# Performance work log

Hardware: AMD Instinct MI355X
Metric: run time of the kernel (lower is better)

Reference implementation:

```python
import jax, jax.numpy as jnp
import numpy as np

B, CIN, COUT, N, K = 4, 64, 64, 16384, 8


def setup_inputs() -> dict:
    key = jax.random.key(0)
    k1, k2, k3, k4, k5 = jax.random.split(key, 5)
    features = jax.random.normal(k1, (B, CIN, N), dtype=jnp.float32)
    neighborhood = jax.random.randint(k2, (B, K, N), 0, N, dtype=jnp.int32)
    positions = jax.random.uniform(k3, (B, 3, N), dtype=jnp.float32)
    # learned parameters (kaiming-uniform-ish init)
    lim_t = np.sqrt(6.0 / CIN)
    weight_theta = jax.random.uniform(k4, (3, CIN, COUT), dtype=jnp.float32,
                                      minval=-lim_t, maxval=lim_t)
    weight_bias = jax.random.uniform(k5, (CIN, COUT), dtype=jnp.float32,
                                     minval=-lim_t, maxval=lim_t)
    bias = jnp.zeros((COUT,), dtype=jnp.float32)
    return {"features": features, "weight_theta": weight_theta,
            "weight_bias": weight_bias, "neighborhood": neighborhood,
            "positions": positions, "bias": bias}


def reference(features, weight_theta, weight_bias, neighborhood, positions, bias):
    # features: [B, Cin, N]; positions: [B, 3, N]; neighborhood: [B, K, N]
    Bv, Cin, Nv = features.shape
    Kv = neighborhood.shape[1]
    # gather neighbor positions: pos_j[b,d,k,n] = positions[b,d, nbh[b,k,n]]
    pos_j = jnp.take_along_axis(positions[:, :, None, :],
                                neighborhood[:, None, :, :].astype(jnp.int32),
                                axis=3)                        # [B,3,K,N]
    delta = pos_j - positions[:, :, None, :]                   # [B,3,K,N]
    # position-dependent linear weight applied to center features:
    # contrib[b,k,o,n] = sum_d delta[b,d,k,n] * (theta.f)[b,d,o,n] + (wb.f)[b,o,n]
    ft = jnp.einsum('dio,bin->bdon', weight_theta, features)   # [B,3,Cout,N]
    fb = jnp.einsum('io,bin->bon', weight_bias, features)      # [B,Cout,N]
    contrib = jnp.einsum('bdkn,bdon->bkon', delta, ft) + fb[:, None]  # [B,K,Cout,N]

    def scatter_b(contrib_b, idx_b):
        # contrib_b: [K,Cout,N], idx_b: [K,N]
        data = contrib_b.transpose(0, 2, 1).reshape(-1, contrib_b.shape[1])  # [K*N, Cout]
        ids = idx_b.reshape(-1)
        return jax.ops.segment_sum(data, ids, num_segments=Nv).T  # [Cout, N]

    out = jax.vmap(scatter_b)(contrib, neighborhood)           # [B,Cout,N]
    return out + bias[None, :, None]
```

## Files before the change

### kernel.cpp

```cpp
#include <hip/hip_runtime.h>
#include <hip/hip_fp16.h>

#define B_    4
#define CIN_  64
#define COUT_ 64
#define N_    16384
#define K_    8

#define EDGES_PER_B (K_ * N_)
#define TOT_EDGES   (B_ * EDGES_PER_B)


__global__ __launch_bounds__(256) void fc_hist(
    const int* __restrict__ nbh,
    int*       __restrict__ counts)
{
    const int gid = blockIdx.x * 256 + threadIdx.x;
    const int b   = gid / EDGES_PER_B;
    const int j   = nbh[gid];
    atomicAdd(&counts[b * N_ + j], 1);
}

__global__ __launch_bounds__(256) void fc_scan(
    const int* __restrict__ counts,
    int*       __restrict__ offsets,
    int*       __restrict__ cursor)
{
    __shared__ int s[256];
    const int b = blockIdx.x;
    const int t = threadIdx.x;
    const int base = b * N_ + t * 64;

    int sum = 0;
    #pragma unroll
    for (int e = 0; e < 64; ++e) sum += counts[base + e];
    s[t] = sum;
    __syncthreads();

    for (int d = 1; d < 256; d <<= 1) {
        const int v = (t >= d) ? s[t - d] : 0;
        __syncthreads();
        s[t] += v;
        __syncthreads();
    }

    int off = s[t] - sum;
    #pragma unroll
    for (int e = 0; e < 64; ++e) {
        const int c = counts[base + e];
        offsets[base + e] = off;
        cursor[base + e]  = off;
        off += c;
    }
}

__global__ __launch_bounds__(256) void fc_rec(
    const int*   __restrict__ nbh,
    const float* __restrict__ pos,
    int*         __restrict__ cursor,
    float4*      __restrict__ rec)
{
    const int gid = blockIdx.x * 256 + threadIdx.x;
    const int b   = gid >> 14;
    const int n   = gid & (N_ - 1);

    const int*   nbhb = nbh + (size_t)b * K_ * N_;
    const float* posb = pos + (size_t)b * 3 * N_;
    float4*      recb = rec + ((size_t)b * N_ + n) * K_;

    #pragma unroll
    for (int k = 0; k < K_; ++k) {
        const int j    = nbhb[k * N_ + n];
        const int slot = atomicAdd(&cursor[b * N_ + j], 1);
        const float qx = posb[j];
        const float qy = posb[N_ + j];
        const float qz = posb[2 * N_ + j];
        recb[k] = make_float4(qx, qy, qz, __int_as_float(slot));
    }
}


__global__ __launch_bounds__(512, 4) void fc_contribA(
    const float*  __restrict__ feat,
    const float*  __restrict__ theta,
    const float*  __restrict__ wbias,
    const float4* __restrict__ rec,
    const float*  __restrict__ pos,
    __half*       __restrict__ contrib)
{
    __shared__ float4 Wl[CIN_ * COUT_];
    __shared__ float  Fl[CIN_ * 64];

    const int tid  = threadIdx.x;
    const int lane = tid & 63;
    const int w    = tid >> 6;

    const int blocks_per_b = N_ / 128;
    const int b     = blockIdx.x / blocks_per_b;
    const int nbase = (blockIdx.x % blocks_per_b) * 128;

    for (int e = tid; e < CIN_ * COUT_; e += 512) {
        const int i = e >> 6, o = e & 63;
        float4 wv;
        wv.x = theta[0 * CIN_ * COUT_ + i * COUT_ + o];
        wv.y = theta[1 * CIN_ * COUT_ + i * COUT_ + o];
        wv.z = theta[2 * CIN_ * COUT_ + i * COUT_ + o];
        wv.w = wbias[i * COUT_ + o];
        Wl[e] = wv;
    }

    const float*  featb = feat + (size_t)b * CIN_ * N_;
    const float*  posb  = pos  + (size_t)b * 3 * N_;
    const float4* recb  = rec  + (size_t)b * N_ * K_;
    __half*       cb    = contrib + ((size_t)b * EDGES_PER_B << 6);

    for (int t = 0; t < 2; ++t) {
        const int n0 = nbase + t * 64;

        __syncthreads();
        for (int r = 0; r < 8; ++r) {
            const int i = r * 8 + w;
            Fl[i * 64 + lane] = featb[(size_t)i * N_ + n0 + lane];
        }
        __syncthreads();

        const int nn = w * 8;
        float4 acc[8];
        #pragma unroll
        for (int j = 0; j < 8; ++j) acc[j] = make_float4(0.f, 0.f, 0.f, 0.f);

        #pragma unroll 2
        for (int i = 0; i < CIN_; ++i) {
            const float4 wv = Wl[i * 64 + lane];
            const float4 fA = *(const float4*)&Fl[i * 64 + nn];
            const float4 fB = *(const float4*)&Fl[i * 64 + nn + 4];
            const float fs[8] = {fA.x, fA.y, fA.z, fA.w, fB.x, fB.y, fB.z, fB.w};
            #pragma unroll
            for (int j = 0; j < 8; ++j) {
                acc[j].x = fmaf(wv.x, fs[j], acc[j].x);
                acc[j].y = fmaf(wv.y, fs[j], acc[j].y);
                acc[j].z = fmaf(wv.z, fs[j], acc[j].z);
                acc[j].w = fmaf(wv.w, fs[j], acc[j].w);
            }
        }

        #pragma unroll
        for (int j = 0; j < 8; ++j) {
            const int n = n0 + nn + j;
            const float px = posb[0 * N_ + n];
            const float py = posb[1 * N_ + n];
            const float pz = posb[2 * N_ + n];
            float4 a = acc[j];
            a.w = fmaf(-px, a.x, fmaf(-py, a.y, fmaf(-pz, a.z, a.w)));
            #pragma unroll
            for (int k = 0; k < K_; ++k) {
                const float4 r = recb[(size_t)n * K_ + k];
                const int slot = __float_as_int(r.w);
                const float c  = fmaf(r.x, a.x, fmaf(r.y, a.y, fmaf(r.z, a.z, a.w)));
                cb[((size_t)slot << 6) + lane] = __float2half(c);
            }
        }
    }
}

struct h4 { __half2 lo, hi; };

__global__ __launch_bounds__(512) void fc_gatherA(
    const __half* __restrict__ contrib,
    const int*    __restrict__ offsets,
    const int*    __restrict__ counts,
    const float*  __restrict__ bias,
    float*        __restrict__ out)
{
    __shared__ float T[64][65];
    __shared__ float V[64][65];
    const int tid  = threadIdx.x;
    const int lane = tid & 63;
    const int w    = tid >> 6;

    const int tiles_per_b = N_ / 64;
    const int b  = blockIdx.x / tiles_per_b;
    const int n0 = (blockIdx.x % tiles_per_b) * 64;

    const __half* cb  = contrib + ((size_t)b * EDGES_PER_B << 6);
    const h4*     cb4 = (const h4*)cb;

    for (int g = 0; g < 8; ++g) {
        const int jj = w * 8 + g;
        const int j  = n0 + jj;
        const int base = offsets[b * N_ + j];
        const int cnt  = counts[b * N_ + j];

        const h4* p4 = cb4 + ((size_t)base << 4) + (lane >> 4) * 16 + (lane & 15);
        float2 sl = make_float2(0.f, 0.f);
        float2 sh = make_float2(0.f, 0.f);
        const int full = cnt >> 2;
        int it = 0;
        for (; it + 2 <= full; it += 2) {
            const h4 a0 = p4[0];
            const h4 a1 = p4[64];
            float2 t0 = __half22float2(a0.lo), t1 = __half22float2(a1.lo);
            sl.x += t0.x + t1.x; sl.y += t0.y + t1.y;
            t0 = __half22float2(a0.hi); t1 = __half22float2(a1.hi);
            sh.x += t0.x + t1.x; sh.y += t0.y + t1.y;
            p4 += 128;
        }
        if (it < full) {
            const h4 a0 = p4[0];
            float2 t0 = __half22float2(a0.lo);
            sl.x += t0.x; sl.y += t0.y;
            t0 = __half22float2(a0.hi);
            sh.x += t0.x; sh.y += t0.y;
        }
        sl.x += __shfl_xor(sl.x, 16); sl.y += __shfl_xor(sl.y, 16);
        sh.x += __shfl_xor(sh.x, 16); sh.y += __shfl_xor(sh.y, 16);
        sl.x += __shfl_xor(sl.x, 32); sl.y += __shfl_xor(sl.y, 32);
        sh.x += __shfl_xor(sh.x, 32); sh.y += __shfl_xor(sh.y, 32);

        float tail = 0.f;
        const __half* pt = cb + (((size_t)(base + (full << 2))) << 6) + lane;
        for (int e = full << 2; e < cnt; ++e) { tail += __half2float(*pt); pt += 64; }

        T[jj][lane] = tail;
        if (lane < 16) {
            V[jj][4 * lane + 0] = sl.x;
            V[jj][4 * lane + 1] = sl.y;
            V[jj][4 * lane + 2] = sh.x;
            V[jj][4 * lane + 3] = sh.y;
        }
    }
    __syncthreads();

    float* outb = out + (size_t)b * COUT_ * N_;
    for (int r = 0; r < 8; ++r) {
        const int o = r * 8 + w;
        outb[(size_t)o * N_ + n0 + lane] = T[lane][o] + V[lane][o] + bias[o];
    }
}


__global__ __launch_bounds__(256) void fc_fill_slot(
    const int* __restrict__ nbh,
    int*       __restrict__ cursor,
    int*       __restrict__ slotmap)
{
    const int gid = blockIdx.x * 256 + threadIdx.x;
    const int b   = gid / EDGES_PER_B;
    const int j   = nbh[gid];
    slotmap[gid] = atomicAdd(&cursor[b * N_ + j], 1);
}

__global__ __launch_bounds__(256) void fc_contrib(
    const float* __restrict__ feat,
    const float* __restrict__ theta,
    const float* __restrict__ wbias,
    const int*   __restrict__ nbh,
    const int*   __restrict__ slotmap,
    const float* __restrict__ pos,
    float*       __restrict__ contrib)
{
    __shared__ float4 Wl[CIN_ * COUT_];
    __shared__ float  Fl[CIN_ * 64];

    const int tid  = threadIdx.x;
    const int lane = tid & 63;
    const int w    = tid >> 6;

    const int blocks_per_b = N_ / 128;
    const int b     = blockIdx.x / blocks_per_b;
    const int nbase = (blockIdx.x % blocks_per_b) * 128;

    for (int e = tid; e < CIN_ * COUT_; e += 256) {
        const int i = e >> 6, o = e & 63;
        float4 wv;
        wv.x = theta[0 * CIN_ * COUT_ + i * COUT_ + o];
        wv.y = theta[1 * CIN_ * COUT_ + i * COUT_ + o];
        wv.z = theta[2 * CIN_ * COUT_ + i * COUT_ + o];
        wv.w = wbias[i * COUT_ + o];
        Wl[e] = wv;
    }

    const float* featb = feat + (size_t)b * CIN_ * N_;
    const float* posb  = pos  + (size_t)b * 3 * N_;
    const int*   nbhb  = nbh  + (size_t)b * K_ * N_;
    const int*   smb   = slotmap + (size_t)b * EDGES_PER_B;
    float*       cb    = contrib + ((size_t)b * EDGES_PER_B << 6);

    for (int t = 0; t < 2; ++t) {
        const int n0 = nbase + t * 64;

        __syncthreads();
        for (int r = 0; r < 16; ++r) {
            const int i = r * 4 + w;
            Fl[i * 64 + lane] = featb[(size_t)i * N_ + n0 + lane];
        }
        __syncthreads();

        for (int g = 0; g < 4; ++g) {
            const int nn = w * 16 + g * 4;
            float4 acc[4];
            #pragma unroll
            for (int j = 0; j < 4; ++j) acc[j] = make_float4(0.f, 0.f, 0.f, 0.f);

            #pragma unroll 8
            for (int i = 0; i < CIN_; ++i) {
                const float4 wv = Wl[i * 64 + lane];
                const float f0 = Fl[i * 64 + nn + 0];
                const float f1 = Fl[i * 64 + nn + 1];
                const float f2 = Fl[i * 64 + nn + 2];
                const float f3 = Fl[i * 64 + nn + 3];
                acc[0].x = fmaf(wv.x, f0, acc[0].x);
                acc[0].y = fmaf(wv.y, f0, acc[0].y);
                acc[0].z = fmaf(wv.z, f0, acc[0].z);
                acc[0].w = fmaf(wv.w, f0, acc[0].w);
                acc[1].x = fmaf(wv.x, f1, acc[1].x);
                acc[1].y = fmaf(wv.y, f1, acc[1].y);
                acc[1].z = fmaf(wv.z, f1, acc[1].z);
                acc[1].w = fmaf(wv.w, f1, acc[1].w);
                acc[2].x = fmaf(wv.x, f2, acc[2].x);
                acc[2].y = fmaf(wv.y, f2, acc[2].y);
                acc[2].z = fmaf(wv.z, f2, acc[2].z);
                acc[2].w = fmaf(wv.w, f2, acc[2].w);
                acc[3].x = fmaf(wv.x, f3, acc[3].x);
                acc[3].y = fmaf(wv.y, f3, acc[3].y);
                acc[3].z = fmaf(wv.z, f3, acc[3].z);
                acc[3].w = fmaf(wv.w, f3, acc[3].w);
            }

            #pragma unroll
            for (int j = 0; j < 4; ++j) {
                const int n = n0 + nn + j;
                const float px = posb[0 * N_ + n];
                const float py = posb[1 * N_ + n];
                const float pz = posb[2 * N_ + n];
                float4 a = acc[j];
                a.w = fmaf(-px, a.x, fmaf(-py, a.y, fmaf(-pz, a.z, a.w)));
                #pragma unroll
                for (int k = 0; k < K_; ++k) {
                    const int jt   = nbhb[k * N_ + n];
                    const int slot = smb[k * N_ + n];
                    const float qx = posb[0 * N_ + jt];
                    const float qy = posb[1 * N_ + jt];
                    const float qz = posb[2 * N_ + jt];
                    const float c  = fmaf(qx, a.x, fmaf(qy, a.y, fmaf(qz, a.z, a.w)));
                    cb[((size_t)slot << 6) + lane] = c;
                }
            }
        }
    }
}

__global__ __launch_bounds__(512) void fc_gather3(
    const float* __restrict__ contrib,
    const int*   __restrict__ offsets,
    const int*   __restrict__ counts,
    const float* __restrict__ bias,
    float*       __restrict__ out)
{
    __shared__ float T[64][65];
    const int tid  = threadIdx.x;
    const int lane = tid & 63;
    const int w    = tid >> 6;

    const int tiles_per_b = N_ / 64;
    const int b  = blockIdx.x / tiles_per_b;
    const int n0 = (blockIdx.x % tiles_per_b) * 64;

    const float* cb = contrib + ((size_t)b * EDGES_PER_B << 6);

    for (int g = 0; g < 8; ++g) {
        const int jj = w * 8 + g;
        const int j  = n0 + jj;
        const int base = offsets[b * N_ + j];
        const int cnt  = counts[b * N_ + j];

        const float* p = cb + ((size_t)base << 6) + lane;
        float acc = 0.f;
        int e = 0;
        for (; e + 4 <= cnt; e += 4) {
            const float v0 = p[0];
            const float v1 = p[64];
            const float v2 = p[128];
            const float v3 = p[192];
            acc += (v0 + v1) + (v2 + v3);
            p += 256;
        }
        for (; e < cnt; ++e) { acc += *p; p += 64; }
        T[jj][lane] = acc;
    }
    __syncthreads();

    float* outb = out + (size_t)b * COUT_ * N_;
    for (int r = 0; r < 8; ++r) {
        const int o = r * 8 + w;
        outb[(size_t)o * N_ + n0 + lane] = T[lane][o] + bias[o];
    }
}

__global__ __launch_bounds__(256) void flexconv_main(
    const float* __restrict__ feat,
    const float* __restrict__ theta,
    const float* __restrict__ wbias,
    const int*   __restrict__ nbh,
    const float* __restrict__ pos,
    float*       __restrict__ ws)
{
    __shared__ float4 Wl[CIN_ * COUT_];
    __shared__ float  Fl[CIN_ * 64];

    const int tid  = threadIdx.x;
    const int lane = tid & 63;
    const int w    = tid >> 6;

    const int blocks_per_b = N_ / 128;
    const int b     = blockIdx.x / blocks_per_b;
    const int nbase = (blockIdx.x % blocks_per_b) * 128;

    for (int e = tid; e < CIN_ * COUT_; e += 256) {
        const int i = e >> 6, o = e & 63;
        float4 wv;
        wv.x = theta[0 * CIN_ * COUT_ + i * COUT_ + o];
        wv.y = theta[1 * CIN_ * COUT_ + i * COUT_ + o];
        wv.z = theta[2 * CIN_ * COUT_ + i * COUT_ + o];
        wv.w = wbias[i * COUT_ + o];
        Wl[e] = wv;
    }

    const float* featb = feat + (size_t)b * CIN_ * N_;
    const float* posb  = pos  + (size_t)b * 3 * N_;
    const int*   nbhb  = nbh  + (size_t)b * K_ * N_;
    float*       wsb   = ws   + (size_t)b * N_ * COUT_;

    for (int t = 0; t < 2; ++t) {
        const int n0 = nbase + t * 64;

        __syncthreads();
        for (int r = 0; r < 16; ++r) {
            const int i = r * 4 + w;
            Fl[i * 64 + lane] = featb[(size_t)i * N_ + n0 + lane];
        }
        __syncthreads();

        for (int g = 0; g < 4; ++g) {
            const int nn = w * 16 + g * 4;
            float4 acc[4];
            #pragma unroll
            for (int j = 0; j < 4; ++j) acc[j] = make_float4(0.f, 0.f, 0.f, 0.f);

            #pragma unroll 8
            for (int i = 0; i < CIN_; ++i) {
                const float4 wv = Wl[i * 64 + lane];
                const float f0 = Fl[i * 64 + nn + 0];
                const float f1 = Fl[i * 64 + nn + 1];
                const float f2 = Fl[i * 64 + nn + 2];
                const float f3 = Fl[i * 64 + nn + 3];
                acc[0].x = fmaf(wv.x, f0, acc[0].x);
                acc[0].y = fmaf(wv.y, f0, acc[0].y);
                acc[0].z = fmaf(wv.z, f0, acc[0].z);
                acc[0].w = fmaf(wv.w, f0, acc[0].w);
                acc[1].x = fmaf(wv.x, f1, acc[1].x);
                acc[1].y = fmaf(wv.y, f1, acc[1].y);
                acc[1].z = fmaf(wv.z, f1, acc[1].z);
                acc[1].w = fmaf(wv.w, f1, acc[1].w);
                acc[2].x = fmaf(wv.x, f2, acc[2].x);
                acc[2].y = fmaf(wv.y, f2, acc[2].y);
                acc[2].z = fmaf(wv.z, f2, acc[2].z);
                acc[2].w = fmaf(wv.w, f2, acc[2].w);
                acc[3].x = fmaf(wv.x, f3, acc[3].x);
                acc[3].y = fmaf(wv.y, f3, acc[3].y);
                acc[3].z = fmaf(wv.z, f3, acc[3].z);
                acc[3].w = fmaf(wv.w, f3, acc[3].w);
            }

            #pragma unroll
            for (int j = 0; j < 4; ++j) {
                const int n = n0 + nn + j;
                const float px = posb[0 * N_ + n];
                const float py = posb[1 * N_ + n];
                const float pz = posb[2 * N_ + n];
                const float4 a = acc[j];
                #pragma unroll
                for (int k = 0; k < K_; ++k) {
                    const int idx = nbhb[k * N_ + n];
                    const float dx = posb[0 * N_ + idx] - px;
                    const float dy = posb[1 * N_ + idx] - py;
                    const float dz = posb[2 * N_ + idx] - pz;
                    const float c  = fmaf(dx, a.x, fmaf(dy, a.y, fmaf(dz, a.z, a.w)));
                    atomicAdd(&wsb[(size_t)idx * COUT_ + lane], c);
                }
            }
        }
    }
}

__global__ __launch_bounds__(256) void flexconv_finish(
    const float* __restrict__ ws,
    const float* __restrict__ bias,
    float*       __restrict__ out)
{
    __shared__ float T[64][65];
    const int tid  = threadIdx.x;
    const int lane = tid & 63;
    const int w    = tid >> 6;

    const int tiles_per_b = N_ / 64;
    const int b  = blockIdx.x / tiles_per_b;
    const int n0 = (blockIdx.x % tiles_per_b) * 64;

    const float* wsb = ws + (size_t)b * N_ * COUT_;
    for (int r = 0; r < 16; ++r) {
        const int nn = r * 4 + w;
        T[nn][lane] = wsb[(size_t)(n0 + nn) * COUT_ + lane];
    }
    __syncthreads();

    float* outb = out + (size_t)b * COUT_ * N_;
    for (int r = 0; r < 16; ++r) {
        const int o = r * 4 + w;
        outb[(size_t)o * N_ + n0 + lane] = T[lane][o] + bias[o];
    }
}

extern "C" void kernel_launch(void* const* d_in, const int* in_sizes, int n_in,
                              void* d_out, int out_size, void* d_ws, size_t ws_size,
                              hipStream_t stream) {
    const float* features = (const float*)d_in[0];
    const float* theta    = (const float*)d_in[1];
    const float* wbias    = (const float*)d_in[2];
    const int*   nbh      = (const int*)  d_in[3];
    const float* pos      = (const float*)d_in[4];
    const float* bias     = (const float*)d_in[5];
    float* out = (float*)d_out;

    const size_t counts_bytes    = (size_t)B_ * N_ * sizeof(int);
    const size_t map_bytes       = (size_t)TOT_EDGES * sizeof(int);
    const size_t rec_bytes       = (size_t)TOT_EDGES * sizeof(float4);
    const size_t contribh_bytes  = (size_t)TOT_EDGES * COUT_ * sizeof(__half);
    const size_t contribf_bytes  = (size_t)TOT_EDGES * COUT_ * sizeof(float);

    {
        size_t off = 0;
        __half* contrib = (__half*)((char*)d_ws + off); off += contribh_bytes;
        int*    offsets = (int*)   ((char*)d_ws + off); off += counts_bytes;
        int*    counts  = (int*)   ((char*)d_ws + off); off += counts_bytes;
        int*    cursor  = (int*)   ((char*)d_ws + off); off += counts_bytes;
        float4* rec     = (float4*)((char*)d_ws + off); off += rec_bytes;

        if (ws_size >= off) {
            hipMemsetAsync(counts, 0, counts_bytes, stream);
            fc_hist<<<TOT_EDGES / 256, 256, 0, stream>>>(nbh, counts);
            fc_scan<<<B_, 256, 0, stream>>>(counts, offsets, cursor);
            fc_rec<<<(B_ * N_) / 256, 256, 0, stream>>>(nbh, pos, cursor, rec);
            fc_contribA<<<B_ * (N_ / 128), 512, 0, stream>>>(features, theta, wbias,
                                                             rec, pos, contrib);
            fc_gatherA<<<B_ * (N_ / 64), 512, 0, stream>>>(contrib, offsets, counts,
                                                           bias, out);
            return;
        }
    }

    {
        size_t off = 0;
        float* contrib = (float*)((char*)d_ws + off); off += contribf_bytes;
        int* counts  = (int*)((char*)d_ws + off); off += counts_bytes;
        int* offsets = (int*)((char*)d_ws + off); off += counts_bytes;
        int* cursor  = (int*)((char*)d_ws + off); off += counts_bytes;
        int* slotmap = (int*)((char*)d_ws + off); off += map_bytes;

        if (ws_size >= off) {
            hipMemsetAsync(counts, 0, counts_bytes, stream);
            fc_hist<<<TOT_EDGES / 256, 256, 0, stream>>>(nbh, counts);
            fc_scan<<<B_, 256, 0, stream>>>(counts, offsets, cursor);
            fc_fill_slot<<<TOT_EDGES / 256, 256, 0, stream>>>(nbh, cursor, slotmap);
            fc_contrib<<<B_ * (N_ / 128), 256, 0, stream>>>(features, theta, wbias,
                                                            nbh, slotmap, pos, contrib);
            fc_gather3<<<B_ * (N_ / 64), 512, 0, stream>>>(contrib, offsets, counts,
                                                           bias, out);
            return;
        }
    }

    {
        float* ws = (float*)d_ws;
        const size_t ws_bytes = (size_t)B_ * N_ * COUT_ * sizeof(float);
        hipMemsetAsync(ws, 0, ws_bytes, stream);
        flexconv_main<<<B_ * (N_ / 128), 256, 0, stream>>>(features, theta, wbias,
                                                           nbh, pos, ws);
        flexconv_finish<<<B_ * (N_ / 64), 256, 0, stream>>>(ws, bias, out);
    }
}
```

Baseline: 190.1 us.

## Fuse all stages into one cooperative persistent kernel with grid syncs

Replaces the memset plus five-kernel pipeline (histogram, scan, record build, contribution, gather) with a single cooperative kernel of 512 blocks. Stages are separated by grid.sync, so per-launch overhead and inter-kernel gaps go away. The gather stage reuses the weight tile's shared memory and handles two tiles per block. Drawbacks are a serial 4-block scan phase while the rest of the grid waits, plus the cost of each grid barrier. If the cooperative launch fails (for example, too many blocks to be co-resident), the code falls back to the old path. The unused fp32 slotmap path is also removed.

Result: slower. 467.3 us (+145.9%).

```diff
diff --git a/kernel.cpp b/kernel.cpp
--- a/kernel.cpp
+++ b/kernel.cpp
@@ -1,5 +1,8 @@
 #include <hip/hip_runtime.h>
 #include <hip/hip_fp16.h>
+#include <hip/hip_cooperative_groups.h>
+
+namespace cg = cooperative_groups;
 
 #define B_    4
 #define CIN_  64
@@ -9,6 +12,228 @@
 
 #define EDGES_PER_B (K_ * N_)
 #define TOT_EDGES   (B_ * EDGES_PER_B)
+
+#define FB 512
+#define FT 512
+
+struct h4 { __half2 lo, hi; };
+
+__global__ __launch_bounds__(512, 4) void fc_fused(
+    const float*  __restrict__ feat,
+    const float*  __restrict__ theta,
+    const float*  __restrict__ wbias,
+    const int*    __restrict__ nbh,
+    const float*  __restrict__ pos,
+    const float*  __restrict__ bias,
+    float*        __restrict__ out,
+    __half*       __restrict__ contrib,
+    int*          __restrict__ offsets,
+    int*          __restrict__ counts,
+    int*          __restrict__ cursor,
+    float4*       __restrict__ rec)
+{
+    __shared__ float4 Wl[CIN_ * COUT_];
+    __shared__ float  Fl[CIN_ * 64];
+
+    cg::grid_group grid = cg::this_grid();
+
+    const int tid = threadIdx.x;
+    const int blk = blockIdx.x;
+    const int gid = blk * FT + tid;
+
+    if (gid < B_ * N_) counts[gid] = 0;
+    grid.sync();
+
+    #pragma unroll
+    for (int r = 0; r < 2; ++r) {
+        const int e = gid + r * (FB * FT);
+        const int b = e / EDGES_PER_B;
+        atomicAdd(&counts[b * N_ + nbh[e]], 1);
+    }
+    grid.sync();
+
+    if (blk < B_) {
+        int* s = (int*)Fl;
+        const int base = blk * N_ + tid * 32;
+        int sum = 0;
+        #pragma unroll
+        for (int q = 0; q < 32; ++q) sum += counts[base + q];
+        s[tid] = sum;
+        __syncthreads();
+        for (int d = 1; d < 512; d <<= 1) {
+            const int v = (tid >= d) ? s[tid - d] : 0;
+            __syncthreads();
+            s[tid] += v;
+            __syncthreads();
+        }
+        int off = s[tid] - sum;
+        #pragma unroll
+        for (int q = 0; q < 32; ++q) {
+            const int c = counts[base + q];
+            offsets[base + q] = off;
+            cursor [base + q] = off;
+            off += c;
+        }
+    }
+    grid.sync();
+
+    if (gid < B_ * N_) {
+        const int b = gid >> 14;
+        const int n = gid & (N_ - 1);
+        const int*   nbhb = nbh + (size_t)b * K_ * N_;
+        const float* posb = pos + (size_t)b * 3 * N_;
+        float4*      recb = rec + ((size_t)b * N_ + n) * K_;
+        #pragma unroll
+        for (int k = 0; k < K_; ++k) {
+            const int j    = nbhb[k * N_ + n];
+            const int slot = atomicAdd(&cursor[b * N_ + j], 1);
+            recb[k] = make_float4(posb[j], posb[N_ + j], posb[2 * N_ + j],
+                                  __int_as_float(slot));
+        }
+    }
+    grid.sync();
+
+    {
+        const int lane = tid & 63;
+        const int w    = tid >> 6;
+        const int b     = blk >> 7;
+        const int nbase = (blk & 127) * 128;
+
+        for (int e = tid; e < CIN_ * COUT_; e += FT) {
+            const int i = e >> 6, o = e & 63;
+            float4 wv;
+            wv.x = theta[0 * CIN_ * COUT_ + i * COUT_ + o];
+            wv.y = theta[1 * CIN_ * COUT_ + i * COUT_ + o];
+            wv.z = theta[2 * CIN_ * COUT_ + i * COUT_ + o];
+            wv.w = wbias[i * COUT_ + o];
+            Wl[e] = wv;
+        }
+
+        const float*  featb = feat + (size_t)b * CIN_ * N_;
+        const float*  posb  = pos  + (size_t)b * 3 * N_;
+        const float4* recb  = rec  + (size_t)b * N_ * K_;
+        __half*       cb    = contrib + ((size_t)b * EDGES_PER_B << 6);
+
+        for (int t = 0; t < 2; ++t) {
+            const int n0 = nbase + t * 64;
+
+            __syncthreads();
+            for (int r = 0; r < 8; ++r) {
+                const int i = r * 8 + w;
+                Fl[i * 64 + lane] = featb[(size_t)i * N_ + n0 + lane];
+            }
+            __syncthreads();
+
+            const int nn = w * 8;
+            float4 acc[8];
+            #pragma unroll
+            for (int j = 0; j < 8; ++j) acc[j] = make_float4(0.f, 0.f, 0.f, 0.f);
+
+            #pragma unroll 2
+            for (int i = 0; i < CIN_; ++i) {
+                const float4 wv = Wl[i * 64 + lane];
+                const float4 fA = *(const float4*)&Fl[i * 64 + nn];
+                const float4 fB = *(const float4*)&Fl[i * 64 + nn + 4];
+                const float fs[8] = {fA.x, fA.y, fA.z, fA.w, fB.x, fB.y, fB.z, fB.w};
+                #pragma unroll
+                for (int j = 0; j < 8; ++j) {
+                    acc[j].x = fmaf(wv.x, fs[j], acc[j].x);
+                    acc[j].y = fmaf(wv.y, fs[j], acc[j].y);
+                    acc[j].z = fmaf(wv.z, fs[j], acc[j].z);
+                    acc[j].w = fmaf(wv.w, fs[j], acc[j].w);
+                }
+            }
+
+            #pragma unroll
+            for (int j = 0; j < 8; ++j) {
+                const int n = n0 + nn + j;
+                const float px = posb[0 * N_ + n];
+                const float py = posb[1 * N_ + n];
+                const float pz = posb[2 * N_ + n];
+                float4 a = acc[j];
+                a.w = fmaf(-px, a.x, fmaf(-py, a.y, fmaf(-pz, a.z, a.w)));
+                #pragma unroll
+                for (int k = 0; k < K_; ++k) {
+                    const float4 r = recb[(size_t)n * K_ + k];
+                    const int slot = __float_as_int(r.w);
+                    const float c  = fmaf(r.x, a.x, fmaf(r.y, a.y, fmaf(r.z, a.z, a.w)));
+                    cb[((size_t)slot << 6) + lane] = __float2half(c);
+                }
+            }
+        }
+    }
+    grid.sync();
+
+    {
+        float (*T)[65] = (float (*)[65])((char*)Wl);
+        float (*V)[65] = (float (*)[65])((char*)Wl + 64 * 65 * sizeof(float));
+        const int lane = tid & 63;
+        const int w    = tid >> 6;
+
+        for (int rep = 0; rep < 2; ++rep) {
+            const int vb = blk + rep * FB;
+            const int b  = vb >> 8;
+            const int n0 = (vb & 255) * 64;
+
+            const __half* cb  = contrib + ((size_t)b * EDGES_PER_B << 6);
+            const h4*     cb4 = (const h4*)cb;
+
+            __syncthreads();
+
+            for (int g = 0; g < 8; ++g) {
+                const int jj = w * 8 + g;
+                const int j  = n0 + jj;
+                const int base = offsets[b * N_ + j];
+                const int cnt  = counts[b * N_ + j];
+
+                const h4* p4 = cb4 + ((size_t)base << 4) + (lane >> 4) * 16 + (lane & 15);
+                float2 sl = make_float2(0.f, 0.f);
+                float2 sh = make_float2(0.f, 0.f);
+                const int full = cnt >> 2;
+                int it = 0;
+                for (; it + 2 <= full; it += 2) {
+                    const h4 a0 = p4[0];
+                    const h4 a1 = p4[64];
+                    float2 t0 = __half22float2(a0.lo), t1 = __half22float2(a1.lo);
+                    sl.x += t0.x + t1.x; sl.y += t0.y + t1.y;
+                    t0 = __half22float2(a0.hi); t1 = __half22float2(a1.hi);
+                    sh.x += t0.x + t1.x; sh.y += t0.y + t1.y;
+                    p4 += 128;
+                }
+                if (it < full) {
+                    const h4 a0 = p4[0];
+                    float2 t0 = __half22float2(a0.lo);
+                    sl.x += t0.x; sl.y += t0.y;
+                    t0 = __half22float2(a0.hi);
+                    sh.x += t0.x; sh.y += t0.y;
+                }
+                sl.x += __shfl_xor(sl.x, 16); sl.y += __shfl_xor(sl.y, 16);
+                sh.x += __shfl_xor(sh.x, 16); sh.y += __shfl_xor(sh.y, 16);
+                sl.x += __shfl_xor(sl.x, 32); sl.y += __shfl_xor(sl.y, 32);
+                sh.x += __shfl_xor(sh.x, 32); sh.y += __shfl_xor(sh.y, 32);
+
+                float tail = 0.f;
+                const __half* pt = cb + (((size_t)(base + (full << 2))) << 6) + lane;
+                for (int e = full << 2; e < cnt; ++e) { tail += __half2float(*pt); pt += 64; }
+
+                T[jj][lane] = tail;
+                if (lane < 16) {
+                    V[jj][4 * lane + 0] = sl.x;
+                    V[jj][4 * lane + 1] = sl.y;
+                    V[jj][4 * lane + 2] = sh.x;
+                    V[jj][4 * lane + 3] = sh.y;
+                }
+            }
+            __syncthreads();
+
+            float* outb = out + (size_t)b * COUT_ * N_;
+            for (int r = 0; r < 8; ++r) {
+                const int o = r * 8 + w;
+                outb[(size_t)o * N_ + n0 + lane] = T[lane][o] + V[lane][o] + bias[o];
+            }
+        }
+    }
+}
 
 
 __global__ __launch_bounds__(256) void fc_hist(
@@ -72,13 +297,10 @@
     for (int k = 0; k < K_; ++k) {
         const int j    = nbhb[k * N_ + n];
         const int slot = atomicAdd(&cursor[b * N_ + j], 1);
-        const float qx = posb[j];
-        const float qy = posb[N_ + j];
-        const float qz = posb[2 * N_ + j];
-        recb[k] = make_float4(qx, qy, qz, __int_as_float(slot));
-    }
-}
-
+        recb[k] = make_float4(posb[j], posb[N_ + j], posb[2 * N_ + j],
+                              __int_as_float(slot));
+    }
+}
 
 __global__ __launch_bounds__(512, 4) void fc_contribA(
     const float*  __restrict__ feat,
@@ -163,8 +385,6 @@
     }
 }
 
-struct h4 { __half2 lo, hi; };
-
 __global__ __launch_bounds__(512) void fc_gatherA(
     const __half* __restrict__ contrib,
     const int*    __restrict__ offsets,
@@ -238,26 +458,13 @@
     }
 }
 
-
-__global__ __launch_bounds__(256) void fc_fill_slot(
-    const int* __restrict__ nbh,
-    int*       __restrict__ cursor,
-    int*       __restrict__ slotmap)
-{
-    const int gid = blockIdx.x * 256 + threadIdx.x;
-    const int b   = gid / EDGES_PER_B;
-    const int j   = nbh[gid];
-    slotmap[gid] = atomicAdd(&cursor[b * N_ + j], 1);
-}
-
-__global__ __launch_bounds__(256) void fc_contrib(
+__global__ __launch_bounds__(256) void flexconv_main(
     const float* __restrict__ feat,
     const float* __restrict__ theta,
     const float* __restrict__ wbias,
     const int*   __restrict__ nbh,
-    const int*   __restrict__ slotmap,
     const float* __restrict__ pos,
-    float*       __restrict__ contrib)
+    float*       __restrict__ ws)
 {
     __shared__ float4 Wl[CIN_ * COUT_];
     __shared__ float  Fl[CIN_ * 64];
@@ -283,8 +490,7 @@
     const float* featb = feat + (size_t)b * CIN_ * N_;
     const float* posb  = pos  + (size_t)b * 3 * N_;
     const int*   nbhb  = nbh  + (size_t)b * K_ * N_;
-    const int*   smb   = slotmap + (size_t)b * EDGES_PER_B;
-    float*       cb    = contrib + ((size_t)b * EDGES_PER_B << 6);
+    float*       wsb   = ws   + (size_t)b * N_ * COUT_;
 
     for (int t = 0; t < 2; ++t) {
         const int n0 = nbase + t * 64;
@@ -333,151 +539,6 @@
                 const float px = posb[0 * N_ + n];
                 const float py = posb[1 * N_ + n];
                 const float pz = posb[2 * N_ + n];
-                float4 a = acc[j];
-                a.w = fmaf(-px, a.x, fmaf(-py, a.y, fmaf(-pz, a.z, a.w)));
-                #pragma unroll
-                for (int k = 0; k < K_; ++k) {
-                    const int jt   = nbhb[k * N_ + n];
-                    const int slot = smb[k * N_ + n];
-                    const float qx = posb[0 * N_ + jt];
-                    const float qy = posb[1 * N_ + jt];
-                    const float qz = posb[2 * N_ + jt];
-                    const float c  = fmaf(qx, a.x, fmaf(qy, a.y, fmaf(qz, a.z, a.w)));
-                    cb[((size_t)slot << 6) + lane] = c;
-                }
-            }
-        }
-    }
-}
-
-__global__ __launch_bounds__(512) void fc_gather3(
-    const float* __restrict__ contrib,
-    const int*   __restrict__ offsets,
-    const int*   __restrict__ counts,
-    const float* __restrict__ bias,
-    float*       __restrict__ out)
-{
-    __shared__ float T[64][65];
-    const int tid  = threadIdx.x;
-    const int lane = tid & 63;
-    const int w    = tid >> 6;
-
-    const int tiles_per_b = N_ / 64;
-    const int b  = blockIdx.x / tiles_per_b;
-    const int n0 = (blockIdx.x % tiles_per_b) * 64;
-
-    const float* cb = contrib + ((size_t)b * EDGES_PER_B << 6);
-
-    for (int g = 0; g < 8; ++g) {
-        const int jj = w * 8 + g;
-        const int j  = n0 + jj;
-        const int base = offsets[b * N_ + j];
-        const int cnt  = counts[b * N_ + j];
-
-        const float* p = cb + ((size_t)base << 6) + lane;
-        float acc = 0.f;
-        int e = 0;
-        for (; e + 4 <= cnt; e += 4) {
-            const float v0 = p[0];
-            const float v1 = p[64];
-            const float v2 = p[128];
-            const float v3 = p[192];
-            acc += (v0 + v1) + (v2 + v3);
-            p += 256;
-        }
-        for (; e < cnt; ++e) { acc += *p; p += 64; }
-        T[jj][lane] = acc;
-    }
-    __syncthreads();
-
-    float* outb = out + (size_t)b * COUT_ * N_;
-    for (int r = 0; r < 8; ++r) {
-        const int o = r * 8 + w;
-        outb[(size_t)o * N_ + n0 + lane] = T[lane][o] + bias[o];
-    }
-}
-
-__global__ __launch_bounds__(256) void flexconv_main(
-    const float* __restrict__ feat,
-    const float* __restrict__ theta,
-    const float* __restrict__ wbias,
-    const int*   __restrict__ nbh,
-    const float* __restrict__ pos,
-    float*       __restrict__ ws)
-{
-    __shared__ float4 Wl[CIN_ * COUT_];
-    __shared__ float  Fl[CIN_ * 64];
-
-    const int tid  = threadIdx.x;
-    const int lane = tid & 63;
-    const int w    = tid >> 6;
-
-    const int blocks_per_b = N_ / 128;
-    const int b     = blockIdx.x / blocks_per_b;
-    const int nbase = (blockIdx.x % blocks_per_b) * 128;
-
-    for (int e = tid; e < CIN_ * COUT_; e += 256) {
-        const int i = e >> 6, o = e & 63;
-        float4 wv;
-        wv.x = theta[0 * CIN_ * COUT_ + i * COUT_ + o];
-        wv.y = theta[1 * CIN_ * COUT_ + i * COUT_ + o];
-        wv.z = theta[2 * CIN_ * COUT_ + i * COUT_ + o];
-        wv.w = wbias[i * COUT_ + o];
-        Wl[e] = wv;
-    }
-
-    const float* featb = feat + (size_t)b * CIN_ * N_;
-    const float* posb  = pos  + (size_t)b * 3 * N_;
-    const int*   nbhb  = nbh  + (size_t)b * K_ * N_;
-    float*       wsb   = ws   + (size_t)b * N_ * COUT_;
-
-    for (int t = 0; t < 2; ++t) {
-        const int n0 = nbase + t * 64;
-
-        __syncthreads();
-        for (int r = 0; r < 16; ++r) {
-            const int i = r * 4 + w;
-            Fl[i * 64 + lane] = featb[(size_t)i * N_ + n0 + lane];
-        }
-        __syncthreads();
-
-        for (int g = 0; g < 4; ++g) {
-            const int nn = w * 16 + g * 4;
-            float4 acc[4];
-            #pragma unroll
-            for (int j = 0; j < 4; ++j) acc[j] = make_float4(0.f, 0.f, 0.f, 0.f);
-
-            #pragma unroll 8
-            for (int i = 0; i < CIN_; ++i) {
-                const float4 wv = Wl[i * 64 + lane];
-                const float f0 = Fl[i * 64 + nn + 0];
-                const float f1 = Fl[i * 64 + nn + 1];
-                const float f2 = Fl[i * 64 + nn + 2];
-                const float f3 = Fl[i * 64 + nn + 3];
-                acc[0].x = fmaf(wv.x, f0, acc[0].x);
-                acc[0].y = fmaf(wv.y, f0, acc[0].y);
-                acc[0].z = fmaf(wv.z, f0, acc[0].z);
-                acc[0].w = fmaf(wv.w, f0, acc[0].w);
-                acc[1].x = fmaf(wv.x, f1, acc[1].x);
-                acc[1].y = fmaf(wv.y, f1, acc[1].y);
-                acc[1].z = fmaf(wv.z, f1, acc[1].z);
-                acc[1].w = fmaf(wv.w, f1, acc[1].w);
-                acc[2].x = fmaf(wv.x, f2, acc[2].x);
-                acc[2].y = fmaf(wv.y, f2, acc[2].y);
-                acc[2].z = fmaf(wv.z, f2, acc[2].z);
-                acc[2].w = fmaf(wv.w, f2, acc[2].w);
-                acc[3].x = fmaf(wv.x, f3, acc[3].x);
-                acc[3].y = fmaf(wv.y, f3, acc[3].y);
-                acc[3].z = fmaf(wv.z, f3, acc[3].z);
-                acc[3].w = fmaf(wv.w, f3, acc[3].w);
-            }
-
-            #pragma unroll
-            for (int j = 0; j < 4; ++j) {
-                const int n = n0 + nn + j;
-                const float px = posb[0 * N_ + n];
-                const float py = posb[1 * N_ + n];
-                const float pz = posb[2 * N_ + n];
                 const float4 a = acc[j];
                 #pragma unroll
                 for (int k = 0; k < K_; ++k) {
@@ -532,11 +593,9 @@
     const float* bias     = (const float*)d_in[5];
     float* out = (float*)d_out;
 
-    const size_t counts_bytes    = (size_t)B_ * N_ * sizeof(int);
-    const size_t map_bytes       = (size_t)TOT_EDGES * sizeof(int);
-    const size_t rec_bytes       = (size_t)TOT_EDGES * sizeof(float4);
-    const size_t contribh_bytes  = (size_t)TOT_EDGES * COUT_ * sizeof(__half);
-    const size_t contribf_bytes  = (size_t)TOT_EDGES * COUT_ * sizeof(float);
+    const size_t counts_bytes   = (size_t)B_ * N_ * sizeof(int);
+    const size_t rec_bytes      = (size_t)TOT_EDGES * sizeof(float4);
+    const size_t contribh_bytes = (size_t)TOT_EDGES * COUT_ * sizeof(__half);
 
     {
         size_t off = 0;
@@ -547,6 +606,16 @@
         float4* rec     = (float4*)((char*)d_ws + off); off += rec_bytes;
 
         if (ws_size >= off) {
+            void* args[] = {
+                (void*)&features, (void*)&theta, (void*)&wbias, (void*)&nbh,
+                (void*)&pos, (void*)&bias, (void*)&out,
+                (void*)&contrib, (void*)&offsets, (void*)&counts,
+                (void*)&cursor, (void*)&rec
+            };
+            hipError_t err = hipLaunchCooperativeKernel(
+                (const void*)fc_fused, dim3(FB), dim3(FT), args, 0, stream);
+            if (err == hipSuccess) return;
+
             hipMemsetAsync(counts, 0, counts_bytes, stream);
             fc_hist<<<TOT_EDGES / 256, 256, 0, stream>>>(nbh, counts);
             fc_scan<<<B_, 256, 0, stream>>>(counts, offsets, cursor);
@@ -560,27 +629,6 @@
     }
 
     {
-        size_t off = 0;
-        float* contrib = (float*)((char*)d_ws + off); off += contribf_bytes;
-        int* counts  = (int*)((char*)d_ws + off); off += counts_bytes;
-        int* offsets = (int*)((char*)d_ws + off); off += counts_bytes;
-        int* cursor  = (int*)((char*)d_ws + off); off += counts_bytes;
-        int* slotmap = (int*)((char*)d_ws + off); off += map_bytes;
-
-        if (ws_size >= off) {
-            hipMemsetAsync(counts, 0, counts_bytes, stream);
-            fc_hist<<<TOT_EDGES / 256, 256, 0, stream>>>(nbh, counts);
-            fc_scan<<<B_, 256, 0, stream>>>(counts, offsets, cursor);
-            fc_fill_slot<<<TOT_EDGES / 256, 256, 0, stream>>>(nbh, cursor, slotmap);
-            fc_contrib<<<B_ * (N_ / 128), 256, 0, stream>>>(features, theta, wbias,
-                                                            nbh, slotmap, pos, contrib);
-            fc_gather3<<<B_ * (N_ / 64), 512, 0, stream>>>(contrib, offsets, counts,
-                                                           bias, out);
-            return;
-        }
-    }
-
-    {
         float* ws = (float*)d_ws;
         const size_t ws_bytes = (size_t)B_ * N_ * COUT_ * sizeof(float);
         hipMemsetAsync(ws, 0, ws_bytes, stream);
```
